# Kernel tuning notes

Measured on AMD Instinct MI355X. Metric: run time of the kernel, lower is better.

## Reference

```python
import jax, jax.numpy as jnp
import numpy as np

GROUPS = 16
KS = 3
EPS = 1e-5  # torch InstanceNorm2d default


def _leaky(x):
    return jnp.where(x > 0, x, 0.1 * x)


def setup_inputs() -> dict:
    key = jax.random.key(0)
    ks = jax.random.split(key, 9)
    B, C, H, W = 8, 256, 128, 128
    R = 512
    s = 0.05
    return {
        "x": jax.random.normal(ks[0], (B, C, H, W), jnp.float32),
        "representation": jax.random.normal(ks[1], (B, R), jnp.float32),
        # SConv.compress_key: Linear(R, C*3*3, bias=False)
        "w_key": jax.random.normal(ks[2], (C * KS * KS, R), jnp.float32) * s,
        # SRAdaIN gamma/beta Linears (R -> C, no bias)
        "w_gamma": jax.random.normal(ks[3], (C, R), jnp.float32) * s,
        "w_beta": jax.random.normal(ks[4], (C, R), jnp.float32) * s,
        # SCM: 1x1 convs R -> R/4 -> C (no bias), PReLU single param init 0.25
        "w_ca1": jax.random.normal(ks[5], (R // 4, R), jnp.float32) * s,
        "prelu_a": jnp.float32(0.25),
        "w_ca2": jax.random.normal(ks[6], (C, R // 4), jnp.float32) * s,
        # ConvLayer: 1x1 conv C -> C with bias
        "w_conv2": jax.random.normal(ks[7], (C, C), jnp.float32) * s,
        "b_conv2": jax.random.normal(ks[8], (C,), jnp.float32) * s,
    }


def reference(x, representation, w_key, w_gamma, w_beta, w_ca1, prelu_a, w_ca2, w_conv2, b_conv2):
    b, c_in, h, w = x.shape
    c_out = w_conv2.shape[0]
    fpg = c_in // GROUPS  # features per group

    # ---- SConv: per-sample dynamic grouped conv (reflection pad, valid conv) ----
    xp = jnp.pad(x, ((0, 0), (0, 0), (1, 1), (1, 1)), mode='reflect')
    # kernel: (b, c_out, 1, 3, 3) then repeat_interleave over in-per-group dim
    kern = _leaky(representation @ w_key.T).reshape(b, c_out, 1, KS, KS)
    kern = jnp.broadcast_to(kern, (b, c_out, fpg, KS, KS))

    def one_conv(xi, ki):
        # xi: (c_in, h+2, w+2); ki: (c_out, fpg, 3, 3)
        return jax.lax.conv_general_dilated(
            xi[None], ki, (1, 1), 'VALID',
            feature_group_count=GROUPS,
            dimension_numbers=('NCHW', 'OIHW', 'NCHW'))[0]

    out = jax.vmap(one_conv)(xp, kern)  # (b, c_out, h, w)

    # ---- SRAdaIN: instance norm (biased var) + learned affine from rep ----
    mean = out.mean(axis=(2, 3), keepdims=True)
    var = out.var(axis=(2, 3), keepdims=True)
    gamma = _leaky(representation @ w_gamma.T)[:, :, None, None]
    beta = _leaky(representation @ w_beta.T)[:, :, None, None]
    out = (out - mean) * jax.lax.rsqrt(var + EPS) * gamma + beta
    out = jax.nn.relu(out)

    # ---- SCM: channel attention gating of the residual ----
    hmid = representation @ w_ca1.T
    hmid = jnp.where(hmid > 0, hmid, prelu_a * hmid)  # PReLU
    att = jax.nn.sigmoid(hmid @ w_ca2.T)[:, :, None, None]  # (b, c_out, 1, 1)
    out = out + x * att

    # ---- ConvLayer: 1x1 conv with bias (pad=0) ----
    out = jnp.einsum('bchw,oc->bohw', out, w_conv2) + b_conv2[None, :, None, None]
    return out
```

## Files before the change

kernel.cpp:

```cpp
#include <hip/hip_runtime.h>
#include <hip/hip_bf16.h>

#define NB 8
#define NC 256
#define NH 128
#define NW 128
#define NR 512
#define NGROUPS 16
#define HP 130
#define NPIX (NH*NW)

#define OFF_KERN  0
#define OFF_GAMMA 18432
#define OFF_BETA  20480
#define OFF_ATT   22528
#define OFF_A     24576
#define OFF_B2    26624
#define OFF_HMID  28672
#define OFF_P     29696
#define OFF_GP    94208
#define OFF_APACK 2257408
#define OFF_PART  2322944

typedef __attribute__((ext_vector_type(8))) short bf16x8;
typedef __attribute__((ext_vector_type(4))) float f32x4;

__device__ __forceinline__ float leakyf(float v) { return v > 0.f ? v : 0.1f * v; }

__device__ __forceinline__ unsigned short f2bf(float f) {
    unsigned u = __float_as_uint(f);
    unsigned r = (u + 0x7FFFu + ((u >> 16) & 1u)) >> 16;
    return (unsigned short)r;
}
__device__ __forceinline__ float bf2f(unsigned short s) {
    return __uint_as_float(((unsigned)s) << 16);
}

__global__ __launch_bounds__(256) void k_params(
    const float* __restrict__ rep, const float* __restrict__ w_key,
    const float* __restrict__ w_gamma, const float* __restrict__ w_beta,
    const float* __restrict__ w_ca1, const float* __restrict__ prelu_a,
    float* __restrict__ ws)
{
    __shared__ float rep_s[NR];
    const int b = blockIdx.y, t = threadIdx.x;
    rep_s[t]       = rep[b*NR + t];
    rep_s[t + 256] = rep[b*NR + t + 256];
    __syncthreads();

    const int r = blockIdx.x * 64 + (t >> 2);
    const int part = t & 3;
    const float* wrow;
    if (r < 2304)      wrow = w_key   + (size_t)r * NR;
    else if (r < 2560) wrow = w_gamma + (size_t)(r - 2304) * NR;
    else if (r < 2816) wrow = w_beta  + (size_t)(r - 2560) * NR;
    else               wrow = w_ca1   + (size_t)(r - 2816) * NR;

    const float4* w4 = (const float4*)wrow + part*32;
    const float4* r4 = (const float4*)rep_s + part*32;
    float acc = 0.f;
    #pragma unroll
    for (int i = 0; i < 32; i++) {
        float4 a = r4[i], w = w4[i];
        acc += a.x*w.x + a.y*w.y + a.z*w.z + a.w*w.w;
    }
    acc += __shfl_xor(acc, 1, 64);
    acc += __shfl_xor(acc, 2, 64);

    if (part == 0) {
        if (r < 2816) {
            const float v = leakyf(acc);
            if (r < 2304)      ws[OFF_KERN  + b*NC*9 + r]        = v;
            else if (r < 2560) ws[OFF_GAMMA + b*NC + r - 2304]   = v;
            else               ws[OFF_BETA  + b*NC + r - 2560]   = v;
        } else {
            const float pa = prelu_a[0];
            ws[OFF_HMID + b*128 + r - 2816] = acc > 0.f ? acc : pa * acc;
        }
    }
}

__global__ __launch_bounds__(256) void k_pack(
    const float* __restrict__ W, float* __restrict__ ws)
{
    const int idx = blockIdx.x * 256 + threadIdx.x;
    const int j    = idx & 7;
    const int lane = (idx >> 3) & 63;
    const int mt   = (idx >> 9) & 15;
    const int ks   = idx >> 13;
    const int m = mt*16 + (lane & 15);
    const int k = ks*32 + (lane >> 4)*8 + j;
    unsigned short* ap = (unsigned short*)(ws + OFF_APACK);
    ap[((ks*16 + mt)*64 + lane)*8 + j] = f2bf(W[m*NC + k]);
}

__global__ __launch_bounds__(256) void k_gsum(
    const float* __restrict__ x, float* __restrict__ ws)
{
    const int bid = blockIdx.x;
    const int pair = bid % 65;
    const int bg = bid / 65;
    const int t = threadIdx.x;
    const int half = t >> 7, tt = t & 127;
    const int yy = pair*2 + half;
    int sy = yy - 1; if (sy < 0) sy = -sy; if (sy > NH-1) sy = 2*(NH-1) - sy;
    const float* xbase = x + (size_t)bg * 16 * NPIX + (size_t)sy * NW;
    float* gp = ws + OFF_GP + ((size_t)bg * HP + yy) * HP;
    for (int xx = tt; xx < HP; xx += 128) {
        int sx = xx - 1; if (sx < 0) sx = -sx; if (sx > NW-1) sx = 2*(NW-1) - sx;
        float s = 0.f;
        #pragma unroll
        for (int k = 0; k < 16; k++) s += xbase[(size_t)k * NPIX + sx];
        gp[xx] = s;
    }
}

__global__ __launch_bounds__(256) void k_stats(float* __restrict__ ws)
{
    const int g = blockIdx.x, b = blockIdx.y, chunk = blockIdx.z, t = threadIdx.x;
    __shared__ float kern_s[16*9];
    __shared__ float red[256*32];
    if (t < 144) kern_s[t] = ws[OFF_KERN + (b*NC + g*16)*9 + t];
    __syncthreads();

    float s[16], q[16];
    #pragma unroll
    for (int i = 0; i < 16; i++) { s[i] = 0.f; q[i] = 0.f; }

    const float* gp = ws + OFF_GP + (size_t)(b*16 + g) * HP * HP;
    const int p0b = chunk * 4096;
    for (int pi = 0; pi < 16; pi++) {
        const int p = p0b + pi*256 + t;
        const int y = p >> 7, xc = p & 127;
        const float* pa = gp + y*HP + xc;
        const float p0 = pa[0],    p1 = pa[1],      p2 = pa[2];
        const float p3 = pa[HP],   p4 = pa[HP+1],   p5 = pa[HP+2];
        const float p6 = pa[2*HP], p7 = pa[2*HP+1], p8 = pa[2*HP+2];
        #pragma unroll
        for (int ch = 0; ch < 16; ch++) {
            const float* k9 = kern_s + ch*9;
            float v = k9[0]*p0 + k9[1]*p1 + k9[2]*p2
                    + k9[3]*p3 + k9[4]*p4 + k9[5]*p5
                    + k9[6]*p6 + k9[7]*p7 + k9[8]*p8;
            s[ch] += v; q[ch] += v*v;
        }
    }
    #pragma unroll
    for (int ch = 0; ch < 16; ch++) { red[t*32 + ch] = s[ch]; red[t*32 + 16 + ch] = q[ch]; }
    for (int st = 128; st >= 1; st >>= 1) {
        __syncthreads();
        if (t < st) {
            #pragma unroll
            for (int v = 0; v < 32; v++) red[t*32 + v] += red[(t+st)*32 + v];
        }
    }
    __syncthreads();
    if (t < 32) {
        ws[OFF_PART + (size_t)((b*16 + g)*4 + chunk)*32 + t] = red[t];
    }
}

__global__ __launch_bounds__(256) void k_fin(
    const float* __restrict__ w_ca2, float* __restrict__ ws)
{
    __shared__ float hm_s[128];
    const int b = blockIdx.x, c = threadIdx.x;
    if (c < 128) hm_s[c] = ws[OFF_HMID + b*128 + c];
    float* P = ws + OFF_P + ((size_t)(b*NC + c) << 4);
    {
        const int g = c >> 4, ch = c & 15;
        const float* part = ws + OFF_PART + (size_t)(b*16 + g)*4*32;
        float S = 0.f, Q = 0.f;
        #pragma unroll
        for (int k = 0; k < 4; k++) { S += part[k*32 + ch]; Q += part[k*32 + 16 + ch]; }
        const float mean = S * (1.f/16384.f);
        const float var  = Q * (1.f/16384.f) - mean*mean;
        const float inv  = rsqrtf(var + 1e-5f);
        const float ga = ws[OFF_GAMMA + b*NC + c];
        const float be = ws[OFF_BETA  + b*NC + c];
        const float a  = ga * inv;
        #pragma unroll
        for (int k = 0; k < 9; k++) P[k] = ws[OFF_KERN + (b*NC + c)*9 + k];
        P[9]  = a;
        P[10] = be - mean * a;
    }
    __syncthreads();
    {
        const float4* w4 = (const float4*)(w_ca2 + c*128);
        const float4* h4 = (const float4*)hm_s;
        float acc = 0.f;
        #pragma unroll
        for (int i = 0; i < 32; i++) {
            float4 a = h4[i], w = w4[i];
            acc += a.x*w.x + a.y*w.y + a.z*w.z + a.w*w.w;
        }
        P[11] = 1.f / (1.f + expf(-acc));
    }
}

__global__ __launch_bounds__(256) void k_main(
    const float* __restrict__ x, const float* __restrict__ ws,
    const float* __restrict__ bias, float* __restrict__ out)
{
    __shared__ unsigned short z_t[64*256];
    __shared__ float4 P_s[NC*3];
    __shared__ float bias_s[NC];

    const int t = threadIdx.x;
    const int wave = t >> 6, lane = t & 63;
    const int x0 = blockIdx.x * 64, y = blockIdx.y, b = blockIdx.z;

    bias_s[t] = bias[t];

    {
        const float4* Pg = (const float4*)(ws + OFF_P + ((size_t)(b*NC) << 4));
        #pragma unroll
        for (int i = 0; i < 3; i++) {
            const int idx = t + i*256;
            const int c = idx / 3, k = idx - c*3;
            P_s[idx] = Pg[c*4 + k];
        }
    }

    char* zb = (char*)z_t;

    const float* gpB = ws + OFF_GP + (size_t)b * 16 * HP * HP;
    const float* xB  = x + (size_t)(b*NC + wave*64) * NPIX + (size_t)y * NW + x0 + lane;

    float xa[8], xb2[8];
    float pA[9], pB[9];
    #pragma unroll
    for (int j = 0; j < 8; j++) xa[j] = xB[(size_t)j * NPIX];
    {
        const float* gpr = gpB + ((size_t)(wave*4) * HP + y) * HP + x0 + lane;
        pA[0]=gpr[0];    pA[1]=gpr[1];      pA[2]=gpr[2];
        pA[3]=gpr[HP];   pA[4]=gpr[HP+1];   pA[5]=gpr[HP+2];
        pA[6]=gpr[2*HP]; pA[7]=gpr[2*HP+1]; pA[8]=gpr[2*HP+2];
    }
    __syncthreads();

    #pragma unroll
    for (int gi = 0; gi < 4; gi++) {
        if (gi < 3) {
            const float* gpr = gpB + ((size_t)(wave*4 + gi + 1) * HP + y) * HP + x0 + lane;
            #pragma unroll
            for (int k = 0; k < 9; k++) {
                const float v = gpr[(k/3)*HP + (k%3)];
                if (gi & 1) pA[k] = v; else pB[k] = v;
            }
        }
        #pragma unroll
        for (int ii2 = 0; ii2 < 2; ii2++) {
            const int ii = gi*2 + ii2;
            if (ii < 7) {
                #pragma unroll
                for (int j = 0; j < 8; j++) {
                    const float v = xB[(size_t)((ii + 1)*8 + j) * NPIX];
                    if (ii & 1) xa[j] = v; else xb2[j] = v;
                }
            }
            bf16x8 zp;
            #pragma unroll
            for (int j = 0; j < 8; j++) {
                const int c = wave*64 + ii*8 + j;
                const float4 q0 = P_s[c*3 + 0];
                const float4 q1 = P_s[c*3 + 1];
                const float4 q2 = P_s[c*3 + 2];
                const float g0 = (gi & 1) ? pB[0] : pA[0], g1 = (gi & 1) ? pB[1] : pA[1];
                const float g2 = (gi & 1) ? pB[2] : pA[2], g3 = (gi & 1) ? pB[3] : pA[3];
                const float g4 = (gi & 1) ? pB[4] : pA[4], g5 = (gi & 1) ? pB[5] : pA[5];
                const float g6 = (gi & 1) ? pB[6] : pA[6], g7 = (gi & 1) ? pB[7] : pA[7];
                const float g8 = (gi & 1) ? pB[8] : pA[8];
                const float conv = g0*q0.x + g1*q0.y + g2*q0.z + g3*q0.w
                                 + g4*q1.x + g5*q1.y + g6*q1.z + g7*q1.w
                                 + g8*q2.x;
                const float xv = (ii & 1) ? xb2[j] : xa[j];
                const float z = fmaxf(fmaf(q2.y, conv, q2.z), 0.f) + xv * q2.w;
                zp[j] = (short)f2bf(z);
            }
            const int c0 = wave*64 + ii*8;
            *(bf16x8*)(zb + lane*512 + ((c0*2) ^ ((lane & 7) << 4))) = zp;
        }
    }
    __syncthreads();

    const unsigned short* ap = (const unsigned short*)(ws + OFF_APACK);
    f32x4 acc[4][4];
    #pragma unroll
    for (int mi = 0; mi < 4; mi++)
        #pragma unroll
        for (int ni = 0; ni < 4; ni++)
            acc[mi][ni] = (f32x4){0.f, 0.f, 0.f, 0.f};

    #pragma unroll
    for (int ks = 0; ks < 8; ks++) {
        bf16x8 bfr[4];
        #pragma unroll
        for (int ni = 0; ni < 4; ni++) {
            const int px = ni*16 + (lane & 15);
            bfr[ni] = *(const bf16x8*)(zb + px*512 + ((ks*64 + (lane >> 4)*16) ^ ((px & 7) << 4)));
        }
        #pragma unroll
        for (int mi = 0; mi < 4; mi++) {
            const bf16x8 afr = *(const bf16x8*)(ap + ((size_t)((ks*16 + wave*4 + mi))*64 + lane)*8);
            #pragma unroll
            for (int ni = 0; ni < 4; ni++)
                acc[mi][ni] = __builtin_amdgcn_mfma_f32_16x16x32_bf16(afr, bfr[ni], acc[mi][ni], 0, 0, 0);
        }
    }

    #pragma unroll
    for (int mi = 0; mi < 4; mi++) {
        const int o_base = wave*64 + mi*16 + (lane >> 4)*4;
        #pragma unroll
        for (int ni = 0; ni < 4; ni++) {
            const int px = x0 + ni*16 + (lane & 15);
            #pragma unroll
            for (int r = 0; r < 4; r++) {
                const int o = o_base + r;
                out[((size_t)(b*NC + o) * NH + y) * NW + px] = acc[mi][ni][r] + bias_s[o];
            }
        }
    }
}

extern "C" void kernel_launch(void* const* d_in, const int* in_sizes, int n_in,
                              void* d_out, int out_size, void* d_ws, size_t ws_size,
                              hipStream_t stream) {
    const float* x       = (const float*)d_in[0];
    const float* rep     = (const float*)d_in[1];
    const float* w_key   = (const float*)d_in[2];
    const float* w_gamma = (const float*)d_in[3];
    const float* w_beta  = (const float*)d_in[4];
    const float* w_ca1   = (const float*)d_in[5];
    const float* prelu_a = (const float*)d_in[6];
    const float* w_ca2   = (const float*)d_in[7];
    const float* w_conv2 = (const float*)d_in[8];
    const float* b_conv2 = (const float*)d_in[9];
    float* out = (float*)d_out;
    float* ws  = (float*)d_ws;

    k_params<<<dim3(46, NB), 256, 0, stream>>>(rep, w_key, w_gamma, w_beta, w_ca1, prelu_a, ws);
    k_pack<<<256, 256, 0, stream>>>(w_conv2, ws);
    k_gsum<<<NB*NGROUPS*65, 256, 0, stream>>>(x, ws);
    k_stats<<<dim3(NGROUPS, NB, 4), 256, 0, stream>>>(ws);
    k_fin<<<NB, 256, 0, stream>>>(w_ca2, ws);
    k_main<<<dim3(2, NH, NB), 256, 0, stream>>>(x, ws, b_conv2, out);
}
```

Measured before the change: 135.4 us.

## Split main kernel pixel tile into two 32-pixel phases to halve LDS and accumulators

The main kernel now processes its 64-pixel row segment in two phases of 32 pixels. In each phase every wave covers 32 channels by 32 pixels, so the LDS staging buffer shrinks from 64x256 to 32x256 bf16 and the MFMA accumulator array from 4x4 to 4x2 tiles. The intent is to cut LDS and register use so more blocks fit per CU and hide memory latency better. In exchange each block needs extra barriers, reloads the A-operand weights from global once per phase, and issues narrower global loads (half-wave 32-float rows) and stores.

```diff
diff --git a/kernel.cpp b/kernel.cpp
--- a/kernel.cpp
+++ b/kernel.cpp
@@ -202,7 +202,7 @@
     const float* __restrict__ x, const float* __restrict__ ws,
     const float* __restrict__ bias, float* __restrict__ out)
 {
-    __shared__ unsigned short z_t[64*256];
+    __shared__ unsigned short z_t[32*256];
     __shared__ float4 P_s[NC*3];
     __shared__ float bias_s[NC];
 
@@ -224,35 +224,37 @@
 
     char* zb = (char*)z_t;
 
+    const int csub = lane >> 5;
+    const int pxl  = lane & 31;
+    const int cw   = wave*64 + csub*32;
     const float* gpB = ws + OFF_GP + (size_t)b * 16 * HP * HP;
-    const float* xB  = x + (size_t)(b*NC + wave*64) * NPIX + (size_t)y * NW + x0 + lane;
-
-    float xa[8], xb2[8];
-    float pA[9], pB[9];
+    const unsigned short* ap = (const unsigned short*)(ws + OFF_APACK);
+
+    __syncthreads();
+
     #pragma unroll
-    for (int j = 0; j < 8; j++) xa[j] = xB[(size_t)j * NPIX];
-    {
-        const float* gpr = gpB + ((size_t)(wave*4) * HP + y) * HP + x0 + lane;
-        pA[0]=gpr[0];    pA[1]=gpr[1];      pA[2]=gpr[2];
-        pA[3]=gpr[HP];   pA[4]=gpr[HP+1];   pA[5]=gpr[HP+2];
-        pA[6]=gpr[2*HP]; pA[7]=gpr[2*HP+1]; pA[8]=gpr[2*HP+2];
-    }
-    __syncthreads();
-
-    #pragma unroll
-    for (int gi = 0; gi < 4; gi++) {
-        if (gi < 3) {
-            const float* gpr = gpB + ((size_t)(wave*4 + gi + 1) * HP + y) * HP + x0 + lane;
-            #pragma unroll
-            for (int k = 0; k < 9; k++) {
-                const float v = gpr[(k/3)*HP + (k%3)];
-                if (gi & 1) pA[k] = v; else pB[k] = v;
-            }
-        }
-        #pragma unroll
-        for (int ii2 = 0; ii2 < 2; ii2++) {
-            const int ii = gi*2 + ii2;
-            if (ii < 7) {
+    for (int ph = 0; ph < 2; ph++) {
+        const int pxg = x0 + ph*32 + pxl;
+        const float* xB = x + (size_t)(b*NC + cw) * NPIX + (size_t)y * NW + pxg;
+
+        float xa[8], xb2[8];
+        float pA[9], pB[9];
+        #pragma unroll
+        for (int j = 0; j < 8; j++) xa[j] = xB[(size_t)j * NPIX];
+        {
+            const float* gpr = gpB + ((size_t)(cw >> 4) * HP + y) * HP + pxg;
+            #pragma unroll
+            for (int k = 0; k < 9; k++) pA[k] = gpr[(k/3)*HP + (k%3)];
+        }
+        {
+            const float* gpr = gpB + ((size_t)((cw >> 4) + 1) * HP + y) * HP + pxg;
+            #pragma unroll
+            for (int k = 0; k < 9; k++) pB[k] = gpr[(k/3)*HP + (k%3)];
+        }
+
+        #pragma unroll
+        for (int ii = 0; ii < 4; ii++) {
+            if (ii < 3) {
                 #pragma unroll
                 for (int j = 0; j < 8; j++) {
                     const float v = xB[(size_t)((ii + 1)*8 + j) * NPIX];
@@ -262,65 +264,64 @@
             bf16x8 zp;
             #pragma unroll
             for (int j = 0; j < 8; j++) {
-                const int c = wave*64 + ii*8 + j;
+                const int c = cw + ii*8 + j;
                 const float4 q0 = P_s[c*3 + 0];
                 const float4 q1 = P_s[c*3 + 1];
                 const float4 q2 = P_s[c*3 + 2];
-                const float g0 = (gi & 1) ? pB[0] : pA[0], g1 = (gi & 1) ? pB[1] : pA[1];
-                const float g2 = (gi & 1) ? pB[2] : pA[2], g3 = (gi & 1) ? pB[3] : pA[3];
-                const float g4 = (gi & 1) ? pB[4] : pA[4], g5 = (gi & 1) ? pB[5] : pA[5];
-                const float g6 = (gi & 1) ? pB[6] : pA[6], g7 = (gi & 1) ? pB[7] : pA[7];
-                const float g8 = (gi & 1) ? pB[8] : pA[8];
-                const float conv = g0*q0.x + g1*q0.y + g2*q0.z + g3*q0.w
-                                 + g4*q1.x + g5*q1.y + g6*q1.z + g7*q1.w
-                                 + g8*q2.x;
+                const bool ub = (ii >= 2);
+                const float conv =
+                      (ub ? pB[0] : pA[0])*q0.x + (ub ? pB[1] : pA[1])*q0.y
+                    + (ub ? pB[2] : pA[2])*q0.z + (ub ? pB[3] : pA[3])*q0.w
+                    + (ub ? pB[4] : pA[4])*q1.x + (ub ? pB[5] : pA[5])*q1.y
+                    + (ub ? pB[6] : pA[6])*q1.z + (ub ? pB[7] : pA[7])*q1.w
+                    + (ub ? pB[8] : pA[8])*q2.x;
                 const float xv = (ii & 1) ? xb2[j] : xa[j];
                 const float z = fmaxf(fmaf(q2.y, conv, q2.z), 0.f) + xv * q2.w;
                 zp[j] = (short)f2bf(z);
             }
-            const int c0 = wave*64 + ii*8;
-            *(bf16x8*)(zb + lane*512 + ((c0*2) ^ ((lane & 7) << 4))) = zp;
-        }
-    }
-    __syncthreads();
-
-    const unsigned short* ap = (const unsigned short*)(ws + OFF_APACK);
-    f32x4 acc[4][4];
-    #pragma unroll
-    for (int mi = 0; mi < 4; mi++)
-        #pragma unroll
-        for (int ni = 0; ni < 4; ni++)
-            acc[mi][ni] = (f32x4){0.f, 0.f, 0.f, 0.f};
-
-    #pragma unroll
-    for (int ks = 0; ks < 8; ks++) {
-        bf16x8 bfr[4];
-        #pragma unroll
-        for (int ni = 0; ni < 4; ni++) {
-            const int px = ni*16 + (lane & 15);
-            bfr[ni] = *(const bf16x8*)(zb + px*512 + ((ks*64 + (lane >> 4)*16) ^ ((px & 7) << 4)));
-        }
+            const int c0 = cw + ii*8;
+            *(bf16x8*)(zb + pxl*512 + ((c0*2) ^ ((pxl & 7) << 4))) = zp;
+        }
+        __syncthreads();
+
+        f32x4 acc[4][2];
         #pragma unroll
         for (int mi = 0; mi < 4; mi++) {
-            const bf16x8 afr = *(const bf16x8*)(ap + ((size_t)((ks*16 + wave*4 + mi))*64 + lane)*8);
-            #pragma unroll
-            for (int ni = 0; ni < 4; ni++)
-                acc[mi][ni] = __builtin_amdgcn_mfma_f32_16x16x32_bf16(afr, bfr[ni], acc[mi][ni], 0, 0, 0);
-        }
-    }
-
-    #pragma unroll
-    for (int mi = 0; mi < 4; mi++) {
-        const int o_base = wave*64 + mi*16 + (lane >> 4)*4;
-        #pragma unroll
-        for (int ni = 0; ni < 4; ni++) {
-            const int px = x0 + ni*16 + (lane & 15);
-            #pragma unroll
-            for (int r = 0; r < 4; r++) {
-                const int o = o_base + r;
-                out[((size_t)(b*NC + o) * NH + y) * NW + px] = acc[mi][ni][r] + bias_s[o];
-            }
-        }
+            acc[mi][0] = (f32x4){0.f, 0.f, 0.f, 0.f};
+            acc[mi][1] = (f32x4){0.f, 0.f, 0.f, 0.f};
+        }
+
+        #pragma unroll
+        for (int ks = 0; ks < 8; ks++) {
+            bf16x8 bfr[2];
+            #pragma unroll
+            for (int ni = 0; ni < 2; ni++) {
+                const int pxc = ni*16 + (lane & 15);
+                bfr[ni] = *(const bf16x8*)(zb + pxc*512 + ((ks*64 + (lane >> 4)*16) ^ ((pxc & 7) << 4)));
+            }
+            #pragma unroll
+            for (int mi = 0; mi < 4; mi++) {
+                const bf16x8 afr = *(const bf16x8*)(ap + ((size_t)((ks*16 + wave*4 + mi))*64 + lane)*8);
+                #pragma unroll
+                for (int ni = 0; ni < 2; ni++)
+                    acc[mi][ni] = __builtin_amdgcn_mfma_f32_16x16x32_bf16(afr, bfr[ni], acc[mi][ni], 0, 0, 0);
+            }
+        }
+
+        #pragma unroll
+        for (int mi = 0; mi < 4; mi++) {
+            const int o_base = wave*64 + mi*16 + (lane >> 4)*4;
+            #pragma unroll
+            for (int ni = 0; ni < 2; ni++) {
+                const int px = x0 + ph*32 + ni*16 + (lane & 15);
+                #pragma unroll
+                for (int r = 0; r < 4; r++) {
+                    const int o = o_base + r;
+                    out[((size_t)(b*NC + o) * NH + y) * NW + px] = acc[mi][ni][r] + bias_s[o];
+                }
+            }
+        }
+        __syncthreads();
     }
 }
 
```

New measurement: 201.2 us. 48.5% more time.
